# Kernel optimization log

Measured on AMD Instinct MI355X. Metric: run time of the kernel, lower is better.

The kernel has to match this reference:

```python
import jax, jax.numpy as jnp
import numpy as np

B, N, C, M = 8, 65536, 64, 64


def _build_frequency_lattice(num_modes: int) -> np.ndarray:
    candidates = []
    radius = 1
    while len(candidates) < num_modes * 2:
        for kx in range(-radius, radius + 1):
            for ky in range(-radius, radius + 1):
                if kx == 0 and ky == 0:
                    continue
                candidates.append((abs(kx) + abs(ky), kx, ky))
        radius += 1
    candidates.sort(key=lambda it: (it[0], abs(it[1]), abs(it[2]), it[1], it[2]))
    unique, seen = [], set()
    for _, kx, ky in candidates:
        if (kx, ky) in seen:
            continue
        seen.add((kx, ky))
        unique.append((kx, ky))
        if len(unique) >= num_modes:
            break
    return np.asarray(unique, dtype=np.float32)  # [M, 2]


def setup_inputs() -> dict:
    key = jax.random.key(0)
    k1, k2, k3, k4 = jax.random.split(key, 4)
    inputs = jax.random.normal(k1, (B, N, C), dtype=jnp.float32)
    coords = jax.random.uniform(k2, (B, N, 2), dtype=jnp.float32)
    scale = 1.0 / C
    # complex weight (M, C) split into real/imag float parts
    weight_re = scale * jax.random.normal(k3, (M, C), dtype=jnp.float32)
    weight_im = scale * jax.random.normal(k4, (M, C), dtype=jnp.float32)
    frequencies = jnp.asarray(_build_frequency_lattice(M))  # [M, 2]
    return {"inputs": inputs, "coords": coords, "weight_re": weight_re,
            "weight_im": weight_im, "frequencies": frequencies}


def reference(inputs, coords, weight_re, weight_im, frequencies):
    # phase: [B, N, M]
    phase = 2.0 * jnp.pi * jnp.einsum('bnc,mc->bnm', coords, frequencies)
    basis = jnp.exp(1j * phase.astype(jnp.complex64))  # [B, N, M]
    # project onto modes: [B, M, C], normalized by N
    coeffs = jnp.einsum('bnm,bnc->bmc', jnp.conj(basis), inputs.astype(jnp.complex64))
    coeffs = coeffs / N
    weight = weight_re + 1j * weight_im  # [M, C]
    mixed = coeffs * weight[None, :, :]  # [B, M, C]
    reconstructed = jnp.einsum('bnm,bmd->bnd', basis, mixed)  # [B, N, C]
    return jnp.real(reconstructed)
```

## Files before the change

kernel.cpp:

```cpp
#include <hip/hip_runtime.h>
#include <hip/hip_bf16.h>

#define BB 8
#define NN 65536
#define CC 64
#define MM 64

typedef __attribute__((ext_vector_type(8))) short bf16x8;
typedef __attribute__((ext_vector_type(4))) float f32x4;
typedef unsigned int u32;
typedef unsigned short u16;

__device__ inline u32 pk_bf2(float a, float b) {
  __hip_bfloat162 h = __float22bfloat162_rn(make_float2(a, b));
  u32 r;
  __builtin_memcpy(&r, &h, 4);
  return r;
}

__device__ inline u16 sbf(float a) {
  __hip_bfloat16 h = __float2bfloat16(a);
  u16 r;
  __builtin_memcpy(&r, &h, 2);
  return r;
}

__device__ inline void rsc(float t, float& sn, float& cs) {
  const float tf = __builtin_amdgcn_fractf(t);
  sn = __builtin_amdgcn_sinf(tf);
  cs = __builtin_amdgcn_cosf(tf);
}

#define CH1 64
#define STEPS1 16

__global__ __launch_bounds__(256) void proj_mfma(
    const float* __restrict__ inputs,
    const float* __restrict__ coords,
    const float* __restrict__ freqs,
    float* __restrict__ partial)
{
  __shared__ __align__(16) u16 As[2][128 * 64];
  __shared__ __align__(16) u16 Xs[2][64 * 64];

  const int tid   = threadIdx.x;
  const int b     = blockIdx.x >> 6;
  const int nbase = (blockIdx.x & 63) * 1024;
  const int lane  = tid & 63;
  const int wave  = tid >> 6;
  const int l15   = lane & 15;
  const int quad  = lane >> 4;

  const int q  = tid & 31;
  const int mg = tid >> 5;
  const int np = tid & 15;
  const int cq = tid >> 4;

  float fqx[8], fqy[8];
#pragma unroll
  for (int mm = 0; mm < 8; ++mm) {
    fqx[mm] = freqs[2 * (mg * 8 + mm)];
    fqy[mm] = freqs[2 * (mg * 8 + mm) + 1];
  }

  const float4* c4 = (const float4*)coords;
  const float4* x4 = (const float4*)inputs;
  const size_t cbase = ((size_t)b * NN + nbase) >> 1;
  const size_t xbase = ((size_t)b * NN + nbase) * 16;

  float4 cs_[2];
  float4 xs_[2][4];

  auto do_load = [&](int s, int slot) {
    cs_[slot] = c4[cbase + (size_t)s * 32 + q];
#pragma unroll
    for (int half = 0; half < 2; ++half) {
      const int n = s * 64 + half * 32 + 2 * np;
      xs_[slot][half * 2 + 0] = x4[xbase + (size_t)n * 16 + cq];
      xs_[slot][half * 2 + 1] = x4[xbase + (size_t)(n + 1) * 16 + cq];
    }
  };

  auto do_stage = [&](int slot, int buf) {
    const float4 cp = cs_[slot];
    const int k8 = q >> 2;
    const int ko = (2 * q) & 7;
#pragma unroll
    for (int mm = 0; mm < 8; ++mm) {
      const int rc = mg * 8 + mm;
      const int rs = rc + 64;
      float s0, c0, s1, c1;
      rsc(fmaf(cp.x, fqx[mm], cp.y * fqy[mm]), s0, c0);
      rsc(fmaf(cp.z, fqx[mm], cp.w * fqy[mm]), s1, c1);
      *(u32*)&As[buf][rc * 64 + ((k8 + rc) & 7) * 8 + ko] = pk_bf2(c0, c1);
      *(u32*)&As[buf][rs * 64 + ((k8 + rs) & 7) * 8 + ko] = pk_bf2(s0, s1);
    }
#pragma unroll
    for (int half = 0; half < 2; ++half) {
      const int k = half * 32 + 2 * np;
      const int k8x = k >> 3, kox = k & 7;
      const float* p0 = (const float*)&xs_[slot][half * 2 + 0];
      const float* p1 = (const float*)&xs_[slot][half * 2 + 1];
#pragma unroll
      for (int j = 0; j < 4; ++j) {
        const int c = cq * 4 + j;
        *(u32*)&Xs[buf][c * 64 + ((k8x + c) & 7) * 8 + kox] = pk_bf2(p0[j], p1[j]);
      }
    }
  };

  f32x4 acc[2][4];
#pragma unroll
  for (int rt = 0; rt < 2; ++rt)
#pragma unroll
    for (int ct = 0; ct < 4; ++ct) acc[rt][ct] = (f32x4){0.f, 0.f, 0.f, 0.f};

  auto do_mfma = [&](int buf) {
#pragma unroll
    for (int kk = 0; kk < 2; ++kk) {
      const int k8q = kk * 4 + quad;
      const int r0 = wave * 32 + l15;
      const int r1 = r0 + 16;
      const bf16x8 a0 = *(const bf16x8*)&As[buf][r0 * 64 + ((k8q + r0) & 7) * 8];
      const bf16x8 a1 = *(const bf16x8*)&As[buf][r1 * 64 + ((k8q + r1) & 7) * 8];
      bf16x8 bfr[4];
#pragma unroll
      for (int ct = 0; ct < 4; ++ct) {
        const int c = ct * 16 + l15;
        bfr[ct] = *(const bf16x8*)&Xs[buf][c * 64 + ((k8q + c) & 7) * 8];
      }
#pragma unroll
      for (int ct = 0; ct < 4; ++ct) {
        acc[0][ct] = __builtin_amdgcn_mfma_f32_16x16x32_bf16(a0, bfr[ct], acc[0][ct], 0, 0, 0);
        acc[1][ct] = __builtin_amdgcn_mfma_f32_16x16x32_bf16(a1, bfr[ct], acc[1][ct], 0, 0, 0);
      }
    }
  };

  do_load(0, 0);
  do_load(1, 1);
  do_stage(0, 0);
  __syncthreads();

#pragma unroll
  for (int s = 0; s < STEPS1; ++s) {
    const int cur = s & 1;
    if (s + 2 < STEPS1) do_load(s + 2, cur);
    do_mfma(cur);
    if (s + 1 < STEPS1) do_stage(1 - cur, 1 - cur);
    __syncthreads();
  }

  float* pb = partial + (size_t)blockIdx.x * (128 * 64);
#pragma unroll
  for (int rt = 0; rt < 2; ++rt)
#pragma unroll
    for (int ct = 0; ct < 4; ++ct)
#pragma unroll
      for (int r = 0; r < 4; ++r) {
        const int mrow = wave * 32 + rt * 16 + quad * 4 + r;
        const int c = ct * 16 + l15;
        pb[mrow * 64 + c] = acc[rt][ct][r];
      }
}

__global__ __launch_bounds__(256) void mix_kernel(
    const float* __restrict__ partial,
    const float* __restrict__ wre, const float* __restrict__ wim,
    u16* __restrict__ w2t)
{
  const int idx = blockIdx.x * 256 + threadIdx.x;
  const int b = idx >> 12;
  const int m = (idx >> 6) & 63;
  const int c = idx & 63;
  const float* pb = partial + (size_t)b * CH1 * 8192;
  float gre = 0.f, gim = 0.f;
#pragma unroll 8
  for (int k = 0; k < CH1; ++k) {
    gre += pb[(size_t)k * 8192 + m * 64 + c];
    gim += pb[(size_t)k * 8192 + (64 + m) * 64 + c];
  }
  const float invN = 1.0f / (float)NN;
  const float wr = wre[m * 64 + c], wi = wim[m * 64 + c];
  u16* wb_ = w2t + (size_t)b * 64 * 128;
  wb_[c * 128 + m]      = sbf((gre * wr + gim * wi) * invN);
  wb_[c * 128 + 64 + m] = sbf((gim * wr - gre * wi) * invN);
}

#define TILES2 8

__global__ __launch_bounds__(256) void recon_mfma(
    const float* __restrict__ coords,
    const u16* __restrict__ w2t,
    const float* __restrict__ freqs,
    float* __restrict__ out)
{
  __shared__ __align__(16) u16 Ps[2][128 * 128];
  __shared__ float sfx[64], sfy[64];

  const int tid   = threadIdx.x;
  const int b     = blockIdx.x >> 6;
  const int nbase = (blockIdx.x & 63) * 1024;
  const int lane  = tid & 63;
  const int wave  = tid >> 6;
  const int l15   = lane & 15;
  const int quad  = lane >> 4;

  if (tid < 64) { sfx[tid] = freqs[2 * tid]; sfy[tid] = freqs[2 * tid + 1]; }

  const int p  = tid & 127;
  const int mg = (tid >> 7) * 32;
  const float2* c2 = (const float2*)coords;
  const size_t cb = (size_t)b * NN + nbase;

  float2 cpre[2];
  cpre[0] = c2[cb + p];
  cpre[1] = c2[cb + 128 + p];

  bf16x8 wb[4][4];
#pragma unroll
  for (int kc = 0; kc < 4; ++kc)
#pragma unroll
    for (int ct = 0; ct < 4; ++ct)
      wb[kc][ct] = *(const bf16x8*)&w2t[((size_t)b * 64 + ct * 16 + l15) * 128 +
                                        kc * 32 + quad * 8];
  __syncthreads();

  auto stage_tile = [&](int buf, float2 cc) {
#pragma unroll
    for (int g = 0; g < 4; ++g) {
      u32 cpk[4], spk[4];
#pragma unroll
      for (int jj = 0; jj < 4; ++jj) {
        const int m = mg + g * 8 + jj * 2;
        float s0, c0, s1, c1;
        rsc(fmaf(cc.x, sfx[m], cc.y * sfy[m]), s0, c0);
        rsc(fmaf(cc.x, sfx[m + 1], cc.y * sfy[m + 1]), s1, c1);
        cpk[jj] = pk_bf2(c0, c1);
        spk[jj] = pk_bf2(s0, s1);
      }
      const int k8c = (mg >> 3) + g;
      const int k8s = k8c + 8;
      *(uint4*)&Ps[buf][p * 128 + ((k8c + p) & 15) * 8] =
          make_uint4(cpk[0], cpk[1], cpk[2], cpk[3]);
      *(uint4*)&Ps[buf][p * 128 + ((k8s + p) & 15) * 8] =
          make_uint4(spk[0], spk[1], spk[2], spk[3]);
    }
  };

  stage_tile(0, cpre[0]);
  __syncthreads();

#pragma unroll
  for (int t = 0; t < TILES2; ++t) {
    const int cur = t & 1;
    if (t + 2 < TILES2) cpre[cur] = c2[cb + (size_t)(t + 2) * 128 + p];

    f32x4 acc[2][4];
#pragma unroll
    for (int rt = 0; rt < 2; ++rt)
#pragma unroll
      for (int ct = 0; ct < 4; ++ct) acc[rt][ct] = (f32x4){0.f, 0.f, 0.f, 0.f};

#pragma unroll
    for (int kc = 0; kc < 4; ++kc) {
      const int k8q = kc * 4 + quad;
      const int r0 = wave * 32 + l15;
      const int r1 = r0 + 16;
      const bf16x8 a0 = *(const bf16x8*)&Ps[cur][r0 * 128 + ((k8q + r0) & 15) * 8];
      const bf16x8 a1 = *(const bf16x8*)&Ps[cur][r1 * 128 + ((k8q + r1) & 15) * 8];
#pragma unroll
      for (int ct = 0; ct < 4; ++ct) {
        acc[0][ct] = __builtin_amdgcn_mfma_f32_16x16x32_bf16(wb[kc][ct], a0, acc[0][ct], 0, 0, 0);
        acc[1][ct] = __builtin_amdgcn_mfma_f32_16x16x32_bf16(wb[kc][ct], a1, acc[1][ct], 0, 0, 0);
      }
    }

    if (t + 1 < TILES2) stage_tile(1 - cur, cpre[1 - cur]);

    float* ob = out + (cb + (size_t)t * 128) * 64;
#pragma unroll
    for (int rt = 0; rt < 2; ++rt)
#pragma unroll
      for (int ct = 0; ct < 4; ++ct) {
        const int n = wave * 32 + rt * 16 + l15;
        *(f32x4*)&ob[(size_t)n * 64 + ct * 16 + quad * 4] = acc[rt][ct];
      }

    __syncthreads();
  }
}

extern "C" void kernel_launch(void* const* d_in, const int* in_sizes, int n_in,
                              void* d_out, int out_size, void* d_ws, size_t ws_size,
                              hipStream_t stream) {
  const float* inputs = (const float*)d_in[0];
  const float* coords = (const float*)d_in[1];
  const float* wre    = (const float*)d_in[2];
  const float* wim    = (const float*)d_in[3];
  const float* freqs  = (const float*)d_in[4];
  float* out = (float*)d_out;

  float* partial = (float*)d_ws;
  u16*   w2t     = (u16*)((char*)d_ws + (size_t)BB * CH1 * 128 * 64 * 4);

  proj_mfma<<<dim3(BB * CH1), dim3(256), 0, stream>>>(inputs, coords, freqs, partial);
  mix_kernel<<<dim3(128), dim3(256), 0, stream>>>(partial, wre, wim, w2t);
  recon_mfma<<<dim3(BB * CH1), dim3(256), 0, stream>>>(coords, w2t, freqs, out);
}
```

Baseline: 263.8 us.

## Generate Fourier basis MFMA fragments directly in registers, bypassing LDS

Both the projection and reconstruction kernels now compute the sin/cos basis values straight into the MFMA operand registers for each lane, instead of staging them through shared memory. This removes the LDS round-trip for the basis matrix, and in recon it also removes all barriers and the double buffer. The cost is redundant work: in projection each lane evaluates both sin and cos but keeps only one, and each thread now loads coordinates from global memory itself. Register pressure is also higher.

Result: slower. 272.8 us (+3.4%).

```diff
diff --git a/kernel.cpp b/kernel.cpp
--- a/kernel.cpp
+++ b/kernel.cpp
@@ -23,6 +23,15 @@
   u16 r;
   __builtin_memcpy(&r, &h, 2);
   return r;
+}
+
+__device__ inline bf16x8 pack8(const float* v) {
+  union { u32 u[4]; bf16x8 f; } r;
+  r.u[0] = pk_bf2(v[0], v[1]);
+  r.u[1] = pk_bf2(v[2], v[3]);
+  r.u[2] = pk_bf2(v[4], v[5]);
+  r.u[3] = pk_bf2(v[6], v[7]);
+  return r.f;
 }
 
 __device__ inline void rsc(float t, float& sn, float& cs) {
@@ -40,7 +49,6 @@
     const float* __restrict__ freqs,
     float* __restrict__ partial)
 {
-  __shared__ __align__(16) u16 As[2][128 * 64];
   __shared__ __align__(16) u16 Xs[2][64 * 64];
 
   const int tid   = threadIdx.x;
@@ -51,28 +59,24 @@
   const int l15   = lane & 15;
   const int quad  = lane >> 4;
 
-  const int q  = tid & 31;
-  const int mg = tid >> 5;
   const int np = tid & 15;
   const int cq = tid >> 4;
 
-  float fqx[8], fqy[8];
-#pragma unroll
-  for (int mm = 0; mm < 8; ++mm) {
-    fqx[mm] = freqs[2 * (mg * 8 + mm)];
-    fqy[mm] = freqs[2 * (mg * 8 + mm) + 1];
-  }
+  const int r0 = wave * 32 + l15;
+  const bool is_sin = (wave >= 2);
+  const int m0 = r0 & 63;
+  const int m1 = m0 + 16;
+  const float fx0 = freqs[2 * m0], fy0 = freqs[2 * m0 + 1];
+  const float fx1 = freqs[2 * m1], fy1 = freqs[2 * m1 + 1];
 
   const float4* c4 = (const float4*)coords;
   const float4* x4 = (const float4*)inputs;
   const size_t cbase = ((size_t)b * NN + nbase) >> 1;
   const size_t xbase = ((size_t)b * NN + nbase) * 16;
 
-  float4 cs_[2];
   float4 xs_[2][4];
 
   auto do_load = [&](int s, int slot) {
-    cs_[slot] = c4[cbase + (size_t)s * 32 + q];
 #pragma unroll
     for (int half = 0; half < 2; ++half) {
       const int n = s * 64 + half * 32 + 2 * np;
@@ -82,19 +86,6 @@
   };
 
   auto do_stage = [&](int slot, int buf) {
-    const float4 cp = cs_[slot];
-    const int k8 = q >> 2;
-    const int ko = (2 * q) & 7;
-#pragma unroll
-    for (int mm = 0; mm < 8; ++mm) {
-      const int rc = mg * 8 + mm;
-      const int rs = rc + 64;
-      float s0, c0, s1, c1;
-      rsc(fmaf(cp.x, fqx[mm], cp.y * fqy[mm]), s0, c0);
-      rsc(fmaf(cp.z, fqx[mm], cp.w * fqy[mm]), s1, c1);
-      *(u32*)&As[buf][rc * 64 + ((k8 + rc) & 7) * 8 + ko] = pk_bf2(c0, c1);
-      *(u32*)&As[buf][rs * 64 + ((k8 + rs) & 7) * 8 + ko] = pk_bf2(s0, s1);
-    }
 #pragma unroll
     for (int half = 0; half < 2; ++half) {
       const int k = half * 32 + 2 * np;
@@ -115,14 +106,31 @@
 #pragma unroll
     for (int ct = 0; ct < 4; ++ct) acc[rt][ct] = (f32x4){0.f, 0.f, 0.f, 0.f};
 
-  auto do_mfma = [&](int buf) {
+  auto make_a = [&](int s, int kk, bf16x8& A0, bf16x8& A1) {
+    float v0[8], v1[8];
+#pragma unroll
+    for (int jj = 0; jj < 4; ++jj) {
+      const float4 cp = c4[cbase + (size_t)s * 32 + kk * 16 + quad * 4 + jj];
+      float s0, c0, s1, c1;
+      rsc(fmaf(cp.x, fx0, cp.y * fy0), s0, c0);
+      rsc(fmaf(cp.z, fx0, cp.w * fy0), s1, c1);
+      v0[2 * jj]     = is_sin ? s0 : c0;
+      v0[2 * jj + 1] = is_sin ? s1 : c1;
+      rsc(fmaf(cp.x, fx1, cp.y * fy1), s0, c0);
+      rsc(fmaf(cp.z, fx1, cp.w * fy1), s1, c1);
+      v1[2 * jj]     = is_sin ? s0 : c0;
+      v1[2 * jj + 1] = is_sin ? s1 : c1;
+    }
+    A0 = pack8(v0);
+    A1 = pack8(v1);
+  };
+
+  auto do_mfma = [&](int buf, int s) {
 #pragma unroll
     for (int kk = 0; kk < 2; ++kk) {
       const int k8q = kk * 4 + quad;
-      const int r0 = wave * 32 + l15;
-      const int r1 = r0 + 16;
-      const bf16x8 a0 = *(const bf16x8*)&As[buf][r0 * 64 + ((k8q + r0) & 7) * 8];
-      const bf16x8 a1 = *(const bf16x8*)&As[buf][r1 * 64 + ((k8q + r1) & 7) * 8];
+      bf16x8 A0, A1;
+      make_a(s, kk, A0, A1);
       bf16x8 bfr[4];
 #pragma unroll
       for (int ct = 0; ct < 4; ++ct) {
@@ -131,8 +139,8 @@
       }
 #pragma unroll
       for (int ct = 0; ct < 4; ++ct) {
-        acc[0][ct] = __builtin_amdgcn_mfma_f32_16x16x32_bf16(a0, bfr[ct], acc[0][ct], 0, 0, 0);
-        acc[1][ct] = __builtin_amdgcn_mfma_f32_16x16x32_bf16(a1, bfr[ct], acc[1][ct], 0, 0, 0);
+        acc[0][ct] = __builtin_amdgcn_mfma_f32_16x16x32_bf16(A0, bfr[ct], acc[0][ct], 0, 0, 0);
+        acc[1][ct] = __builtin_amdgcn_mfma_f32_16x16x32_bf16(A1, bfr[ct], acc[1][ct], 0, 0, 0);
       }
     }
   };
@@ -146,7 +154,7 @@
   for (int s = 0; s < STEPS1; ++s) {
     const int cur = s & 1;
     if (s + 2 < STEPS1) do_load(s + 2, cur);
-    do_mfma(cur);
+    do_mfma(cur, s);
     if (s + 1 < STEPS1) do_stage(1 - cur, 1 - cur);
     __syncthreads();
   }
@@ -195,9 +203,6 @@
     const float* __restrict__ freqs,
     float* __restrict__ out)
 {
-  __shared__ __align__(16) u16 Ps[2][128 * 128];
-  __shared__ float sfx[64], sfy[64];
-
   const int tid   = threadIdx.x;
   const int b     = blockIdx.x >> 6;
   const int nbase = (blockIdx.x & 63) * 1024;
@@ -206,16 +211,13 @@
   const int l15   = lane & 15;
   const int quad  = lane >> 4;
 
-  if (tid < 64) { sfx[tid] = freqs[2 * tid]; sfy[tid] = freqs[2 * tid + 1]; }
-
-  const int p  = tid & 127;
-  const int mg = (tid >> 7) * 32;
-  const float2* c2 = (const float2*)coords;
-  const size_t cb = (size_t)b * NN + nbase;
-
-  float2 cpre[2];
-  cpre[0] = c2[cb + p];
-  cpre[1] = c2[cb + 128 + p];
+  float fxa[8], fya[8], fxb[8], fyb[8];
+#pragma unroll
+  for (int j = 0; j < 8; ++j) {
+    const int ma = quad * 8 + j;
+    fxa[j] = freqs[2 * ma];        fya[j] = freqs[2 * ma + 1];
+    fxb[j] = freqs[2 * (ma + 32)]; fyb[j] = freqs[2 * (ma + 32) + 1];
+  }
 
   bf16x8 wb[4][4];
 #pragma unroll
@@ -224,70 +226,44 @@
     for (int ct = 0; ct < 4; ++ct)
       wb[kc][ct] = *(const bf16x8*)&w2t[((size_t)b * 64 + ct * 16 + l15) * 128 +
                                         kc * 32 + quad * 8];
-  __syncthreads();
-
-  auto stage_tile = [&](int buf, float2 cc) {
-#pragma unroll
-    for (int g = 0; g < 4; ++g) {
-      u32 cpk[4], spk[4];
-#pragma unroll
-      for (int jj = 0; jj < 4; ++jj) {
-        const int m = mg + g * 8 + jj * 2;
-        float s0, c0, s1, c1;
-        rsc(fmaf(cc.x, sfx[m], cc.y * sfy[m]), s0, c0);
-        rsc(fmaf(cc.x, sfx[m + 1], cc.y * sfy[m + 1]), s1, c1);
-        cpk[jj] = pk_bf2(c0, c1);
-        spk[jj] = pk_bf2(s0, s1);
-      }
-      const int k8c = (mg >> 3) + g;
-      const int k8s = k8c + 8;
-      *(uint4*)&Ps[buf][p * 128 + ((k8c + p) & 15) * 8] =
-          make_uint4(cpk[0], cpk[1], cpk[2], cpk[3]);
-      *(uint4*)&Ps[buf][p * 128 + ((k8s + p) & 15) * 8] =
-          make_uint4(spk[0], spk[1], spk[2], spk[3]);
-    }
-  };
-
-  stage_tile(0, cpre[0]);
-  __syncthreads();
+
+  const float2* c2 = (const float2*)coords;
+  const size_t cb = (size_t)b * NN + nbase;
 
 #pragma unroll
   for (int t = 0; t < TILES2; ++t) {
-    const int cur = t & 1;
-    if (t + 2 < TILES2) cpre[cur] = c2[cb + (size_t)(t + 2) * 128 + p];
-
-    f32x4 acc[2][4];
-#pragma unroll
-    for (int rt = 0; rt < 2; ++rt)
-#pragma unroll
-      for (int ct = 0; ct < 4; ++ct) acc[rt][ct] = (f32x4){0.f, 0.f, 0.f, 0.f};
-
-#pragma unroll
-    for (int kc = 0; kc < 4; ++kc) {
-      const int k8q = kc * 4 + quad;
-      const int r0 = wave * 32 + l15;
-      const int r1 = r0 + 16;
-      const bf16x8 a0 = *(const bf16x8*)&Ps[cur][r0 * 128 + ((k8q + r0) & 15) * 8];
-      const bf16x8 a1 = *(const bf16x8*)&Ps[cur][r1 * 128 + ((k8q + r1) & 15) * 8];
-#pragma unroll
-      for (int ct = 0; ct < 4; ++ct) {
-        acc[0][ct] = __builtin_amdgcn_mfma_f32_16x16x32_bf16(wb[kc][ct], a0, acc[0][ct], 0, 0, 0);
-        acc[1][ct] = __builtin_amdgcn_mfma_f32_16x16x32_bf16(wb[kc][ct], a1, acc[1][ct], 0, 0, 0);
-      }
-    }
-
-    if (t + 1 < TILES2) stage_tile(1 - cur, cpre[1 - cur]);
-
     float* ob = out + (cb + (size_t)t * 128) * 64;
 #pragma unroll
-    for (int rt = 0; rt < 2; ++rt)
-#pragma unroll
-      for (int ct = 0; ct < 4; ++ct) {
-        const int n = wave * 32 + rt * 16 + l15;
-        *(f32x4*)&ob[(size_t)n * 64 + ct * 16 + quad * 4] = acc[rt][ct];
-      }
-
-    __syncthreads();
+    for (int rt = 0; rt < 2; ++rt) {
+      const int nl = wave * 32 + rt * 16 + l15;
+      const float2 cc = c2[cb + (size_t)t * 128 + nl];
+
+      float va[8], vb[8], vc[8], vd[8];
+#pragma unroll
+      for (int j = 0; j < 8; ++j) {
+        float s0, c0;
+        rsc(fmaf(cc.x, fxa[j], cc.y * fya[j]), s0, c0);
+        va[j] = c0; vc[j] = s0;
+        rsc(fmaf(cc.x, fxb[j], cc.y * fyb[j]), s0, c0);
+        vb[j] = c0; vd[j] = s0;
+      }
+      bf16x8 pf[4];
+      pf[0] = pack8(va); pf[1] = pack8(vb);
+      pf[2] = pack8(vc); pf[3] = pack8(vd);
+
+      f32x4 acc[4];
+#pragma unroll
+      for (int ct = 0; ct < 4; ++ct) acc[ct] = (f32x4){0.f, 0.f, 0.f, 0.f};
+#pragma unroll
+      for (int kc = 0; kc < 4; ++kc)
+#pragma unroll
+        for (int ct = 0; ct < 4; ++ct)
+          acc[ct] = __builtin_amdgcn_mfma_f32_16x16x32_bf16(wb[kc][ct], pf[kc], acc[ct], 0, 0, 0);
+
+#pragma unroll
+      for (int ct = 0; ct < 4; ++ct)
+        *(f32x4*)&ob[(size_t)nl * 64 + ct * 16 + quad * 4] = acc[ct];
+    }
   }
 }
 
```
